# Kernel tuning notes

Hardware: AMD Instinct MI355X
Metric: run time of the kernel (lower is better)

## Reference

```python
import jax, jax.numpy as jnp
import numpy as np

T, H, E, I, TOP_K = 2048, 1024, 8, 2048, 2
SOFTCAP = 30.0


def setup_inputs() -> dict:
    key = jax.random.key(0)
    k1, k2, k3, k4, k5 = jax.random.split(key, 5)
    scale_h = 1.0 / np.sqrt(H)
    scale_i = 1.0 / np.sqrt(I)
    return {
        "hidden_states": jax.random.normal(k1, (T, H), dtype=jnp.float32),
        "gate_w": jax.random.normal(k2, (H, E), dtype=jnp.float32) * scale_h,
        "wg": jax.random.normal(k3, (E, H, I), dtype=jnp.float32) * scale_h,
        "wu": jax.random.normal(k4, (E, H, I), dtype=jnp.float32) * scale_h,
        "wd": jax.random.normal(k5, (E, I, H), dtype=jnp.float32) * scale_i,
    }


def reference(hidden_states, gate_w, wg, wu, wd):
    # Router: fp32 linear gate, then softcap: logits/cap -> tanh (as in source)
    router_logits = hidden_states @ gate_w                      # [T, E]
    router_logits = jnp.tanh(router_logits / SOFTCAP)

    # Top-k routing: softmax over the selected top-k logits (renormalized)
    topk_vals, topk_idx = jax.lax.top_k(router_logits, TOP_K)    # [T, K]
    topk_probs = jax.nn.softmax(topk_vals, axis=-1)              # [T, K]
    # Dense combine weights [T, E], zero for unselected experts
    weights = jnp.zeros((T, E), dtype=hidden_states.dtype)
    weights = weights.at[jnp.arange(T)[:, None], topk_idx].set(topk_probs)

    # Grouped expert MLP (gated, gelu): out_e = gelu(x@wg_e) * (x@wu_e) @ wd_e
    g = jnp.einsum("th,ehi->tei", hidden_states, wg)             # [T, E, I]
    u = jnp.einsum("th,ehi->tei", hidden_states, wu)             # [T, E, I]
    act = jax.nn.gelu(g) * u                                     # [T, E, I]
    expert_out = jnp.einsum("tei,eih->teh", act, wd)             # [T, E, H]

    # Weighted combine across experts
    return jnp.einsum("te,teh->th", weights, expert_out)         # [T, H]
```

## Files before the change

kernel.cpp:

```cpp
#include <hip/hip_runtime.h>
#include <hip/hip_bf16.h>

#define TT 2048
#define HD 1024
#define NE 8
#define ID 2048

typedef short bf16x8 __attribute__((ext_vector_type(8)));
typedef float f32x4 __attribute__((ext_vector_type(4)));

__device__ __forceinline__ unsigned f2bf(float f){
  unsigned u = __float_as_uint(f);
  return (u + 0x7FFFu + ((u >> 16) & 1u)) >> 16;
}
__device__ __forceinline__ float gelu_t(float x){
  float x3 = x * x * x;
  return 0.5f * x * (1.f + tanhf(0.7978845608028654f * (x + 0.044715f * x3)));
}

typedef const __attribute__((address_space(1))) unsigned int as1_uint;
typedef __attribute__((address_space(3))) unsigned int as3_uint;
__device__ __forceinline__ void gll16(const unsigned short* g, unsigned short* l) {
  __builtin_amdgcn_global_load_lds((as1_uint*)g, (as3_uint*)l, 16, 0, 0);
}

__global__ __launch_bounds__(64) void router_kernel(
    const float* __restrict__ x, const float* __restrict__ gw,
    int* __restrict__ counts, int* __restrict__ list_ak, float* __restrict__ wlist)
{
  int t = blockIdx.x;
  int lane = threadIdx.x;
  float acc[NE];
  #pragma unroll
  for (int e = 0; e < NE; ++e) acc[e] = 0.f;
  const float* xr = x + (size_t)t * HD;
  #pragma unroll
  for (int j = 0; j < HD / 64; ++j) {
    int h = j * 64 + lane;
    float xv = xr[h];
    float4 g0 = *(const float4*)(gw + (size_t)h * NE);
    float4 g1 = *(const float4*)(gw + (size_t)h * NE + 4);
    acc[0] += xv * g0.x; acc[1] += xv * g0.y;
    acc[2] += xv * g0.z; acc[3] += xv * g0.w;
    acc[4] += xv * g1.x; acc[5] += xv * g1.y;
    acc[6] += xv * g1.z; acc[7] += xv * g1.w;
  }
  #pragma unroll
  for (int e = 0; e < NE; ++e) {
    float v = acc[e];
    #pragma unroll
    for (int off = 32; off > 0; off >>= 1) v += __shfl_xor(v, off, 64);
    acc[e] = v;
  }
  if (lane == 0) {
    float lg[NE];
    #pragma unroll
    for (int e = 0; e < NE; ++e) lg[e] = tanhf(acc[e] * (1.0f / 30.0f));
    int i0 = 0;
    #pragma unroll
    for (int e = 1; e < NE; ++e) if (lg[e] > lg[i0]) i0 = e;
    int i1 = (i0 == 0) ? 1 : 0;
    #pragma unroll
    for (int e = 0; e < NE; ++e) if (e != i0 && lg[e] > lg[i1]) i1 = e;
    float e1 = __expf(lg[i1] - lg[i0]);
    float w0 = 1.f / (1.f + e1);
    float w1 = 1.f - w0;
    int p0 = atomicAdd(counts + i0, 1);
    list_ak[i0 * TT + p0] = t * 2;
    wlist[i0 * TT + p0] = w0;
    int p1 = atomicAdd(counts + i1, 1);
    list_ak[i1 * TT + p1] = t * 2 + 1;
    wlist[i1 * TT + p1] = w1;
  }
}

__global__ void xcvt_kernel(const float* __restrict__ x, unsigned short* __restrict__ xb)
{
  int i = blockIdx.x * blockDim.x + threadIdx.x;
  const float* p = x + (size_t)i * 8;
  float4 v0 = *(const float4*)p;
  float4 v1 = *(const float4*)(p + 4);
  uint4 o;
  o.x = f2bf(v0.x) | (f2bf(v0.y) << 16);
  o.y = f2bf(v0.z) | (f2bf(v0.w) << 16);
  o.z = f2bf(v1.x) | (f2bf(v1.y) << 16);
  o.w = f2bf(v1.z) | (f2bf(v1.w) << 16);
  *(uint4*)(xb + (size_t)i * 8) = o;
}

__global__ __launch_bounds__(256) void tcvt_kernel(
    const float* __restrict__ in, unsigned short* __restrict__ out, int R, int C)
{
  __shared__ float tile[64 * 66];
  int e = blockIdx.z;
  const float* inp = in + (size_t)e * R * C;
  unsigned short* outp = out + (size_t)e * R * C;
  int r0 = blockIdx.y * 64, c0 = blockIdx.x * 64;
  int tid = threadIdx.x;
  int lr = tid >> 4, lc = (tid & 15) * 4;
  #pragma unroll
  for (int i = 0; i < 4; ++i) {
    float4 v = *(const float4*)(inp + (size_t)(r0 + i * 16 + lr) * C + c0 + lc);
    float* tp = &tile[(i * 16 + lr) * 66 + lc];
    tp[0] = v.x; tp[1] = v.y; tp[2] = v.z; tp[3] = v.w;
  }
  __syncthreads();
  int oc = tid >> 2, os = (tid & 3) * 16;
  unsigned short* op = outp + (size_t)(c0 + oc) * R + r0 + os;
  uint4 o[2];
  unsigned* ow = (unsigned*)o;
  #pragma unroll
  for (int m = 0; m < 8; ++m) {
    float a = tile[(os + 2 * m) * 66 + oc];
    float b = tile[(os + 2 * m + 1) * 66 + oc];
    ow[m] = f2bf(a) | (f2bf(b) << 16);
  }
  *(uint4*)op = o[0];
  *(uint4*)(op + 8) = o[1];
}

#define BK 32


__global__ __launch_bounds__(256, 4) void gu_gemm(
    const unsigned short* __restrict__ xb,
    const unsigned short* __restrict__ wgT,
    const unsigned short* __restrict__ wuT,
    unsigned short* __restrict__ act,
    const int* __restrict__ counts, const int* __restrict__ list_ak)
{
  int e = blockIdx.z;
  int nCnt = counts[e];
  int m0 = blockIdx.y * 64;
  if (m0 >= nCnt) return;
  int c0 = blockIdx.x * 128;
  const unsigned short* Wg = wgT + (size_t)e * HD * ID;
  const unsigned short* Wu = wuT + (size_t)e * HD * ID;

  __shared__ __align__(16) unsigned short As[2][64 * BK];
  __shared__ __align__(16) unsigned short Bg[2][128 * BK];
  __shared__ __align__(16) unsigned short Bu[2][128 * BK];

  int tid = threadIdx.x;
  int wave = tid >> 6, lane = tid & 63;
  int wn = wave * 32;

  int arow = wave * 16 + (lane >> 2);
  int gpos = m0 + arow; if (gpos >= nCnt) gpos = nCnt - 1;
  int usw = ((lane & 3) ^ ((lane >> 3) & 3)) * 8;
  const unsigned short* aptr =
      xb + (size_t)(list_ak[e * TT + gpos] >> 1) * HD + usw;
  int aldso = wave * 512;

  int colL = wave * 16 + (lane >> 2);
  const unsigned short* bg0 = Wg + (size_t)(c0 + colL) * HD + usw;
  const unsigned short* bu0 = Wu + (size_t)(c0 + colL) * HD + usw;
  const size_t bstep = (size_t)64 * HD;
  int ldso = wave * 512;

  auto stage = [&](int k0, int b) {
    gll16(aptr + k0,         &As[b][aldso]);
    gll16(bg0 + k0,          &Bg[b][ldso]);
    gll16(bg0 + k0 + bstep,  &Bg[b][ldso + 2048]);
    gll16(bu0 + k0,          &Bu[b][ldso]);
    gll16(bu0 + k0 + bstep,  &Bu[b][ldso + 2048]);
  };

  f32x4 accg[4][2], accu[4][2];
  f32x4 zed = {0.f, 0.f, 0.f, 0.f};
  #pragma unroll
  for (int i = 0; i < 4; ++i)
    #pragma unroll
    for (int j = 0; j < 2; ++j) { accg[i][j] = zed; accu[i][j] = zed; }

  stage(0, 0);

  int q = lane >> 4, l15 = lane & 15;
  int bswz = (q ^ ((l15 >> 1) & 3)) * 8;

  for (int k0 = 0; k0 < HD; k0 += BK) {
    int cur = (k0 >> 5) & 1;
    if (k0 + BK < HD) {
      stage(k0 + BK, cur ^ 1);
      asm volatile("s_waitcnt vmcnt(5)" ::: "memory");
    } else {
      asm volatile("s_waitcnt vmcnt(0)" ::: "memory");
    }
    __builtin_amdgcn_s_barrier();

    bf16x8 af[4];
    #pragma unroll
    for (int mt = 0; mt < 4; ++mt) {
      int r = mt * 16 + l15;
      af[mt] = *(const bf16x8*)(&As[cur][r * BK + ((q ^ ((r >> 1) & 3)) * 8)]);
    }
    #pragma unroll
    for (int nt = 0; nt < 2; ++nt) {
      int col = wn + nt * 16 + l15;
      bf16x8 bgf  = *(const bf16x8*)(&Bg[cur][col * BK + bswz]);
      bf16x8 buf_ = *(const bf16x8*)(&Bu[cur][col * BK + bswz]);
      #pragma unroll
      for (int mt = 0; mt < 4; ++mt) {
        accg[mt][nt] = __builtin_amdgcn_mfma_f32_16x16x32_bf16(af[mt], bgf,  accg[mt][nt], 0, 0, 0);
        accu[mt][nt] = __builtin_amdgcn_mfma_f32_16x16x32_bf16(af[mt], buf_, accu[mt][nt], 0, 0, 0);
      }
    }
    asm volatile("s_waitcnt lgkmcnt(0)" ::: "memory");
    __builtin_amdgcn_s_barrier();
  }

  int cc = lane & 15, rg = lane >> 4;
  #pragma unroll
  for (int mt = 0; mt < 4; ++mt) {
    #pragma unroll
    for (int r = 0; r < 4; ++r) {
      int pos = m0 + mt * 16 + rg * 4 + r;
      if (pos >= nCnt) continue;
      int ak = list_ak[e * TT + pos];
      #pragma unroll
      for (int nt = 0; nt < 2; ++nt) {
        int ncol = c0 + wn + nt * 16 + cc;
        float avl = gelu_t(accg[mt][nt][r]) * accu[mt][nt][r];
        act[(size_t)ak * ID + ncol] = (unsigned short)f2bf(avl);
      }
    }
  }
}

__global__ __launch_bounds__(256, 5) void d_gemm(
    const unsigned short* __restrict__ act,
    const unsigned short* __restrict__ wdT,
    float* __restrict__ yw,
    const int* __restrict__ counts, const int* __restrict__ list_ak,
    const float* __restrict__ wlist)
{
  int e = blockIdx.z;
  int nCnt = counts[e];
  int m0 = (blockIdx.y >> 1) * 64;
  int ks = blockIdx.y & 1;
  if (m0 >= nCnt) return;
  int c0 = blockIdx.x * 128;
  const unsigned short* Wd = wdT + (size_t)e * ID * HD;

  __shared__ __align__(16) unsigned short As[2][64 * BK];
  __shared__ __align__(16) unsigned short Bt[2][128 * BK];

  int tid = threadIdx.x;
  int wave = tid >> 6, lane = tid & 63;
  int wn = wave * 32;

  int arow = wave * 16 + (lane >> 2);
  int gpos = m0 + arow; if (gpos >= nCnt) gpos = nCnt - 1;
  int usw = ((lane & 3) ^ ((lane >> 3) & 3)) * 8;
  const unsigned short* aptr =
      act + (size_t)list_ak[e * TT + gpos] * ID + ks * 1024 + usw;
  int aldso = wave * 512;

  int colL = wave * 16 + (lane >> 2);
  const unsigned short* bp0 = Wd + (size_t)(c0 + colL) * ID + ks * 1024 + usw;
  const size_t bstep = (size_t)64 * ID;
  int ldso = wave * 512;

  auto stage = [&](int k0, int b) {
    gll16(aptr + k0,        &As[b][aldso]);
    gll16(bp0 + k0,         &Bt[b][ldso]);
    gll16(bp0 + k0 + bstep, &Bt[b][ldso + 2048]);
  };

  f32x4 acc[4][2];
  f32x4 zed = {0.f, 0.f, 0.f, 0.f};
  #pragma unroll
  for (int i = 0; i < 4; ++i)
    #pragma unroll
    for (int j = 0; j < 2; ++j) acc[i][j] = zed;

  stage(0, 0);

  int q = lane >> 4, l15 = lane & 15;
  int bswz = (q ^ ((l15 >> 1) & 3)) * 8;

  for (int k0 = 0; k0 < 1024; k0 += BK) {
    int cur = (k0 >> 5) & 1;
    if (k0 + BK < 1024) {
      stage(k0 + BK, cur ^ 1);
      asm volatile("s_waitcnt vmcnt(3)" ::: "memory");
    } else {
      asm volatile("s_waitcnt vmcnt(0)" ::: "memory");
    }
    __builtin_amdgcn_s_barrier();

    bf16x8 af[4], bf[2];
    #pragma unroll
    for (int mt = 0; mt < 4; ++mt) {
      int r = mt * 16 + l15;
      af[mt] = *(const bf16x8*)(&As[cur][r * BK + ((q ^ ((r >> 1) & 3)) * 8)]);
    }
    #pragma unroll
    for (int nt = 0; nt < 2; ++nt) {
      int col = wn + nt * 16 + l15;
      bf[nt] = *(const bf16x8*)(&Bt[cur][col * BK + bswz]);
    }
    #pragma unroll
    for (int mt = 0; mt < 4; ++mt)
      #pragma unroll
      for (int nt = 0; nt < 2; ++nt)
        acc[mt][nt] = __builtin_amdgcn_mfma_f32_16x16x32_bf16(af[mt], bf[nt], acc[mt][nt], 0, 0, 0);

    asm volatile("s_waitcnt lgkmcnt(0)" ::: "memory");
    __builtin_amdgcn_s_barrier();
  }

  int cc = lane & 15, rg = lane >> 4;
  #pragma unroll
  for (int mt = 0; mt < 4; ++mt) {
    #pragma unroll
    for (int r = 0; r < 4; ++r) {
      int pos = m0 + mt * 16 + rg * 4 + r;
      if (pos >= nCnt) continue;
      int ak = list_ak[e * TT + pos];
      float wsc = wlist[e * TT + pos];
      #pragma unroll
      for (int nt = 0; nt < 2; ++nt) {
        int ncol = c0 + wn + nt * 16 + cc;
        yw[((size_t)ks * (TT * 2) + ak) * HD + ncol] = acc[mt][nt][r] * wsc;
      }
    }
  }
}

__global__ void combine_kernel(const float* __restrict__ yw, float* __restrict__ out)
{
  const int total = TT * HD / 4;
  const size_t S = (size_t)TT * 2 * HD;
  for (int i = blockIdx.x * blockDim.x + threadIdx.x; i < total;
       i += gridDim.x * blockDim.x) {
    int i4 = i * 4;
    int t = i4 >> 10;
    int h = i4 & (HD - 1);
    float4 a = *(const float4*)(yw + (size_t)(2 * t) * HD + h);
    float4 b = *(const float4*)(yw + (size_t)(2 * t + 1) * HD + h);
    float4 c = *(const float4*)(yw + S + (size_t)(2 * t) * HD + h);
    float4 d = *(const float4*)(yw + S + (size_t)(2 * t + 1) * HD + h);
    float4 o;
    o.x = a.x + b.x + c.x + d.x;
    o.y = a.y + b.y + c.y + d.y;
    o.z = a.z + b.z + c.z + d.z;
    o.w = a.w + b.w + c.w + d.w;
    *(float4*)(out + (size_t)i4) = o;
  }
}

extern "C" void kernel_launch(void* const* d_in, const int* in_sizes, int n_in,
                              void* d_out, int out_size, void* d_ws, size_t ws_size,
                              hipStream_t stream) {
  const float* x  = (const float*)d_in[0];
  const float* gw = (const float*)d_in[1];
  const float* wg = (const float*)d_in[2];
  const float* wu = (const float*)d_in[3];
  const float* wd = (const float*)d_in[4];
  float* out = (float*)d_out;

  char* ws = (char*)d_ws;
  int* counts   = (int*)ws;
  int* list_ak  = (int*)(ws + 256);
  float* wlist  = (float*)(ws + 256 + 65536);
  size_t off = 256 + 2 * 65536;
  unsigned short* xb  = (unsigned short*)(ws + off); off += (size_t)TT * HD * 2;
  unsigned short* act = (unsigned short*)(ws + off); off += (size_t)TT * 2 * ID * 2;
  float* yw           = (float*)(ws + off);          off += (size_t)2 * TT * 2 * HD * 4;
  unsigned short* wgT = (unsigned short*)(ws + off); off += (size_t)NE * HD * ID * 2;
  unsigned short* wuT = (unsigned short*)(ws + off); off += (size_t)NE * HD * ID * 2;
  unsigned short* wdT = (unsigned short*)(ws + off);

  (void)hipMemsetAsync(counts, 0, 256, stream);
  router_kernel<<<TT, 64, 0, stream>>>(x, gw, counts, list_ak, wlist);
  xcvt_kernel<<<TT * HD / 8 / 256, 256, 0, stream>>>(x, xb);

  tcvt_kernel<<<dim3(ID / 64, HD / 64, NE), 256, 0, stream>>>(wg, wgT, HD, ID);
  tcvt_kernel<<<dim3(ID / 64, HD / 64, NE), 256, 0, stream>>>(wu, wuT, HD, ID);
  tcvt_kernel<<<dim3(HD / 64, ID / 64, NE), 256, 0, stream>>>(wd, wdT, ID, HD);

  dim3 blk(256);
  dim3 gGU(ID / 128, 32, NE);
  gu_gemm<<<gGU, blk, 0, stream>>>(xb, wgT, wuT, act, counts, list_ak);

  dim3 gD(HD / 128, 64, NE);
  d_gemm<<<gD, blk, 0, stream>>>(act, wdT, yw, counts, list_ak, wlist);

  combine_kernel<<<1024, 256, 0, stream>>>(yw, out);
}
```

Baseline: 396.8 us.

## Load expert weights directly to registers and use persistent row-strided GEMM blocks

Both expert GEMMs stop staging weight tiles through shared memory. Each wave now loads its B fragments straight from global memory into registers, one k-step ahead, and only the gathered activation rows go through LDS. The grid is reshaped to (expert, 8 or 16 slots, column tiles), and each block loops over row tiles with stride 512 instead of exiting early on empty tiles, which cuts idle blocks and LDS use. The cost is that weight loads are no longer shared across waves through LDS and are strided 16-byte global reads that rely on the caches. The column-tile-major launch order may also change L2 reuse of weights. The d_gemm occupancy hint also drops from 5 to 4.

```diff
diff --git a/kernel.cpp b/kernel.cpp
--- a/kernel.cpp
+++ b/kernel.cpp
@@ -129,200 +129,192 @@
     unsigned short* __restrict__ act,
     const int* __restrict__ counts, const int* __restrict__ list_ak)
 {
-  int e = blockIdx.z;
+  int e = blockIdx.x;
   int nCnt = counts[e];
-  int m0 = blockIdx.y * 64;
-  if (m0 >= nCnt) return;
-  int c0 = blockIdx.x * 128;
+  int c0 = blockIdx.z * 128;
   const unsigned short* Wg = wgT + (size_t)e * HD * ID;
   const unsigned short* Wu = wuT + (size_t)e * HD * ID;
 
   __shared__ __align__(16) unsigned short As[2][64 * BK];
-  __shared__ __align__(16) unsigned short Bg[2][128 * BK];
-  __shared__ __align__(16) unsigned short Bu[2][128 * BK];
 
   int tid = threadIdx.x;
   int wave = tid >> 6, lane = tid & 63;
   int wn = wave * 32;
-
-  int arow = wave * 16 + (lane >> 2);
-  int gpos = m0 + arow; if (gpos >= nCnt) gpos = nCnt - 1;
+  int q = lane >> 4, l15 = lane & 15;
   int usw = ((lane & 3) ^ ((lane >> 3) & 3)) * 8;
-  const unsigned short* aptr =
-      xb + (size_t)(list_ak[e * TT + gpos] >> 1) * HD + usw;
   int aldso = wave * 512;
-
-  int colL = wave * 16 + (lane >> 2);
-  const unsigned short* bg0 = Wg + (size_t)(c0 + colL) * HD + usw;
-  const unsigned short* bu0 = Wu + (size_t)(c0 + colL) * HD + usw;
-  const size_t bstep = (size_t)64 * HD;
-  int ldso = wave * 512;
-
-  auto stage = [&](int k0, int b) {
-    gll16(aptr + k0,         &As[b][aldso]);
-    gll16(bg0 + k0,          &Bg[b][ldso]);
-    gll16(bg0 + k0 + bstep,  &Bg[b][ldso + 2048]);
-    gll16(bu0 + k0,          &Bu[b][ldso]);
-    gll16(bu0 + k0 + bstep,  &Bu[b][ldso + 2048]);
-  };
-
-  f32x4 accg[4][2], accu[4][2];
-  f32x4 zed = {0.f, 0.f, 0.f, 0.f};
-  #pragma unroll
-  for (int i = 0; i < 4; ++i)
-    #pragma unroll
-    for (int j = 0; j < 2; ++j) { accg[i][j] = zed; accu[i][j] = zed; }
-
-  stage(0, 0);
-
-  int q = lane >> 4, l15 = lane & 15;
-  int bswz = (q ^ ((l15 >> 1) & 3)) * 8;
-
-  for (int k0 = 0; k0 < HD; k0 += BK) {
-    int cur = (k0 >> 5) & 1;
-    if (k0 + BK < HD) {
-      stage(k0 + BK, cur ^ 1);
-      asm volatile("s_waitcnt vmcnt(5)" ::: "memory");
-    } else {
-      asm volatile("s_waitcnt vmcnt(0)" ::: "memory");
-    }
-    __builtin_amdgcn_s_barrier();
-
-    bf16x8 af[4];
+  int afsw = (q ^ ((l15 >> 1) & 3)) * 8;
+
+  const unsigned short* pBg = Wg + (size_t)(c0 + wn + l15) * HD + q * 8;
+  const unsigned short* pBu = Wu + (size_t)(c0 + wn + l15) * HD + q * 8;
+  const size_t ntstep = (size_t)16 * HD;
+
+  for (int m0 = blockIdx.y * 64; m0 < nCnt; m0 += 8 * 64) {
+    int gpos = m0 + wave * 16 + (lane >> 2);
+    if (gpos >= nCnt) gpos = nCnt - 1;
+    const unsigned short* aptr =
+        xb + (size_t)(list_ak[e * TT + gpos] >> 1) * HD + usw;
+
+    f32x4 accg[4][2], accu[4][2];
+    f32x4 zed = {0.f, 0.f, 0.f, 0.f};
+    #pragma unroll
+    for (int i = 0; i < 4; ++i)
+      #pragma unroll
+      for (int j = 0; j < 2; ++j) { accg[i][j] = zed; accu[i][j] = zed; }
+
+    bf16x8 bgf[2], buf_[2];
+    gll16(aptr, &As[0][aldso]);
+    #pragma unroll
+    for (int nt = 0; nt < 2; ++nt) {
+      bgf[nt]  = *(const bf16x8*)(pBg + nt * ntstep);
+      buf_[nt] = *(const bf16x8*)(pBu + nt * ntstep);
+    }
+    asm volatile("" ::: "memory");
+
+    for (int k0 = 0; k0 < HD; k0 += BK) {
+      int cur = (k0 >> 5) & 1;
+      int nk = k0 + BK;
+      if (nk < HD) {
+        gll16(aptr + nk, &As[cur ^ 1][aldso]);
+        asm volatile("s_waitcnt vmcnt(1)" ::: "memory");
+      } else {
+        asm volatile("s_waitcnt vmcnt(0)" ::: "memory");
+      }
+      __builtin_amdgcn_s_barrier();
+
+      bf16x8 af[4];
+      #pragma unroll
+      for (int mt = 0; mt < 4; ++mt)
+        af[mt] = *(const bf16x8*)(&As[cur][(mt * 16 + l15) * BK + afsw]);
+
+      #pragma unroll
+      for (int nt = 0; nt < 2; ++nt) {
+        bf16x8 bg = bgf[nt], bu = buf_[nt];
+        #pragma unroll
+        for (int mt = 0; mt < 4; ++mt) {
+          accg[mt][nt] = __builtin_amdgcn_mfma_f32_16x16x32_bf16(af[mt], bg, accg[mt][nt], 0, 0, 0);
+          accu[mt][nt] = __builtin_amdgcn_mfma_f32_16x16x32_bf16(af[mt], bu, accu[mt][nt], 0, 0, 0);
+        }
+        if (nk < HD) {
+          bgf[nt]  = *(const bf16x8*)(pBg + nt * ntstep + nk);
+          buf_[nt] = *(const bf16x8*)(pBu + nt * ntstep + nk);
+        }
+      }
+      asm volatile("s_waitcnt lgkmcnt(0)" ::: "memory");
+      asm volatile("" ::: "memory");
+      __builtin_amdgcn_s_barrier();
+    }
+
+    int cc = lane & 15, rg = lane >> 4;
     #pragma unroll
     for (int mt = 0; mt < 4; ++mt) {
-      int r = mt * 16 + l15;
-      af[mt] = *(const bf16x8*)(&As[cur][r * BK + ((q ^ ((r >> 1) & 3)) * 8)]);
-    }
-    #pragma unroll
-    for (int nt = 0; nt < 2; ++nt) {
-      int col = wn + nt * 16 + l15;
-      bf16x8 bgf  = *(const bf16x8*)(&Bg[cur][col * BK + bswz]);
-      bf16x8 buf_ = *(const bf16x8*)(&Bu[cur][col * BK + bswz]);
-      #pragma unroll
-      for (int mt = 0; mt < 4; ++mt) {
-        accg[mt][nt] = __builtin_amdgcn_mfma_f32_16x16x32_bf16(af[mt], bgf,  accg[mt][nt], 0, 0, 0);
-        accu[mt][nt] = __builtin_amdgcn_mfma_f32_16x16x32_bf16(af[mt], buf_, accu[mt][nt], 0, 0, 0);
-      }
-    }
-    asm volatile("s_waitcnt lgkmcnt(0)" ::: "memory");
-    __builtin_amdgcn_s_barrier();
-  }
-
-  int cc = lane & 15, rg = lane >> 4;
-  #pragma unroll
-  for (int mt = 0; mt < 4; ++mt) {
-    #pragma unroll
-    for (int r = 0; r < 4; ++r) {
-      int pos = m0 + mt * 16 + rg * 4 + r;
-      if (pos >= nCnt) continue;
-      int ak = list_ak[e * TT + pos];
-      #pragma unroll
-      for (int nt = 0; nt < 2; ++nt) {
-        int ncol = c0 + wn + nt * 16 + cc;
-        float avl = gelu_t(accg[mt][nt][r]) * accu[mt][nt][r];
-        act[(size_t)ak * ID + ncol] = (unsigned short)f2bf(avl);
-      }
-    }
-  }
-}
-
-__global__ __launch_bounds__(256, 5) void d_gemm(
+      #pragma unroll
+      for (int r = 0; r < 4; ++r) {
+        int pos = m0 + mt * 16 + rg * 4 + r;
+        if (pos >= nCnt) continue;
+        int ak = list_ak[e * TT + pos];
+        #pragma unroll
+        for (int nt = 0; nt < 2; ++nt) {
+          int ncol = c0 + wn + nt * 16 + cc;
+          float avl = gelu_t(accg[mt][nt][r]) * accu[mt][nt][r];
+          act[(size_t)ak * ID + ncol] = (unsigned short)f2bf(avl);
+        }
+      }
+    }
+  }
+}
+
+__global__ __launch_bounds__(256, 4) void d_gemm(
     const unsigned short* __restrict__ act,
     const unsigned short* __restrict__ wdT,
     float* __restrict__ yw,
     const int* __restrict__ counts, const int* __restrict__ list_ak,
     const float* __restrict__ wlist)
 {
-  int e = blockIdx.z;
+  int e = blockIdx.x;
   int nCnt = counts[e];
-  int m0 = (blockIdx.y >> 1) * 64;
+  int mslot = blockIdx.y >> 1;
   int ks = blockIdx.y & 1;
-  if (m0 >= nCnt) return;
-  int c0 = blockIdx.x * 128;
+  int c0 = blockIdx.z * 128;
   const unsigned short* Wd = wdT + (size_t)e * ID * HD;
 
   __shared__ __align__(16) unsigned short As[2][64 * BK];
-  __shared__ __align__(16) unsigned short Bt[2][128 * BK];
 
   int tid = threadIdx.x;
   int wave = tid >> 6, lane = tid & 63;
   int wn = wave * 32;
-
-  int arow = wave * 16 + (lane >> 2);
-  int gpos = m0 + arow; if (gpos >= nCnt) gpos = nCnt - 1;
+  int q = lane >> 4, l15 = lane & 15;
   int usw = ((lane & 3) ^ ((lane >> 3) & 3)) * 8;
-  const unsigned short* aptr =
-      act + (size_t)list_ak[e * TT + gpos] * ID + ks * 1024 + usw;
   int aldso = wave * 512;
-
-  int colL = wave * 16 + (lane >> 2);
-  const unsigned short* bp0 = Wd + (size_t)(c0 + colL) * ID + ks * 1024 + usw;
-  const size_t bstep = (size_t)64 * ID;
-  int ldso = wave * 512;
-
-  auto stage = [&](int k0, int b) {
-    gll16(aptr + k0,        &As[b][aldso]);
-    gll16(bp0 + k0,         &Bt[b][ldso]);
-    gll16(bp0 + k0 + bstep, &Bt[b][ldso + 2048]);
-  };
-
-  f32x4 acc[4][2];
-  f32x4 zed = {0.f, 0.f, 0.f, 0.f};
-  #pragma unroll
-  for (int i = 0; i < 4; ++i)
-    #pragma unroll
-    for (int j = 0; j < 2; ++j) acc[i][j] = zed;
-
-  stage(0, 0);
-
-  int q = lane >> 4, l15 = lane & 15;
-  int bswz = (q ^ ((l15 >> 1) & 3)) * 8;
-
-  for (int k0 = 0; k0 < 1024; k0 += BK) {
-    int cur = (k0 >> 5) & 1;
-    if (k0 + BK < 1024) {
-      stage(k0 + BK, cur ^ 1);
-      asm volatile("s_waitcnt vmcnt(3)" ::: "memory");
-    } else {
-      asm volatile("s_waitcnt vmcnt(0)" ::: "memory");
-    }
-    __builtin_amdgcn_s_barrier();
-
-    bf16x8 af[4], bf[2];
+  int afsw = (q ^ ((l15 >> 1) & 3)) * 8;
+
+  const unsigned short* pB = Wd + (size_t)(c0 + wn + l15) * ID + ks * 1024 + q * 8;
+  const size_t ntstep = (size_t)16 * ID;
+
+  for (int m0 = mslot * 64; m0 < nCnt; m0 += 8 * 64) {
+    int gpos = m0 + wave * 16 + (lane >> 2);
+    if (gpos >= nCnt) gpos = nCnt - 1;
+    const unsigned short* aptr =
+        act + (size_t)list_ak[e * TT + gpos] * ID + ks * 1024 + usw;
+
+    f32x4 acc[4][2];
+    f32x4 zed = {0.f, 0.f, 0.f, 0.f};
+    #pragma unroll
+    for (int i = 0; i < 4; ++i)
+      #pragma unroll
+      for (int j = 0; j < 2; ++j) acc[i][j] = zed;
+
+    bf16x8 bf[2];
+    gll16(aptr, &As[0][aldso]);
+    #pragma unroll
+    for (int nt = 0; nt < 2; ++nt)
+      bf[nt] = *(const bf16x8*)(pB + nt * ntstep);
+    asm volatile("" ::: "memory");
+
+    for (int k0 = 0; k0 < 1024; k0 += BK) {
+      int cur = (k0 >> 5) & 1;
+      int nk = k0 + BK;
+      if (nk < 1024) {
+        gll16(aptr + nk, &As[cur ^ 1][aldso]);
+        asm volatile("s_waitcnt vmcnt(1)" ::: "memory");
+      } else {
+        asm volatile("s_waitcnt vmcnt(0)" ::: "memory");
+      }
+      __builtin_amdgcn_s_barrier();
+
+      bf16x8 af[4];
+      #pragma unroll
+      for (int mt = 0; mt < 4; ++mt)
+        af[mt] = *(const bf16x8*)(&As[cur][(mt * 16 + l15) * BK + afsw]);
+
+      #pragma unroll
+      for (int nt = 0; nt < 2; ++nt) {
+        bf16x8 b = bf[nt];
+        #pragma unroll
+        for (int mt = 0; mt < 4; ++mt)
+          acc[mt][nt] = __builtin_amdgcn_mfma_f32_16x16x32_bf16(af[mt], b, acc[mt][nt], 0, 0, 0);
+        if (nk < 1024)
+          bf[nt] = *(const bf16x8*)(pB + nt * ntstep + nk);
+      }
+      asm volatile("s_waitcnt lgkmcnt(0)" ::: "memory");
+      asm volatile("" ::: "memory");
+      __builtin_amdgcn_s_barrier();
+    }
+
+    int cc = lane & 15, rg = lane >> 4;
     #pragma unroll
     for (int mt = 0; mt < 4; ++mt) {
-      int r = mt * 16 + l15;
-      af[mt] = *(const bf16x8*)(&As[cur][r * BK + ((q ^ ((r >> 1) & 3)) * 8)]);
-    }
-    #pragma unroll
-    for (int nt = 0; nt < 2; ++nt) {
-      int col = wn + nt * 16 + l15;
-      bf[nt] = *(const bf16x8*)(&Bt[cur][col * BK + bswz]);
-    }
-    #pragma unroll
-    for (int mt = 0; mt < 4; ++mt)
-      #pragma unroll
-      for (int nt = 0; nt < 2; ++nt)
-        acc[mt][nt] = __builtin_amdgcn_mfma_f32_16x16x32_bf16(af[mt], bf[nt], acc[mt][nt], 0, 0, 0);
-
-    asm volatile("s_waitcnt lgkmcnt(0)" ::: "memory");
-    __builtin_amdgcn_s_barrier();
-  }
-
-  int cc = lane & 15, rg = lane >> 4;
-  #pragma unroll
-  for (int mt = 0; mt < 4; ++mt) {
-    #pragma unroll
-    for (int r = 0; r < 4; ++r) {
-      int pos = m0 + mt * 16 + rg * 4 + r;
-      if (pos >= nCnt) continue;
-      int ak = list_ak[e * TT + pos];
-      float wsc = wlist[e * TT + pos];
-      #pragma unroll
-      for (int nt = 0; nt < 2; ++nt) {
-        int ncol = c0 + wn + nt * 16 + cc;
-        yw[((size_t)ks * (TT * 2) + ak) * HD + ncol] = acc[mt][nt][r] * wsc;
+      #pragma unroll
+      for (int r = 0; r < 4; ++r) {
+        int pos = m0 + mt * 16 + rg * 4 + r;
+        if (pos >= nCnt) continue;
+        int ak = list_ak[e * TT + pos];
+        float wsc = wlist[e * TT + pos];
+        #pragma unroll
+        for (int nt = 0; nt < 2; ++nt) {
+          int ncol = c0 + wn + nt * 16 + cc;
+          yw[((size_t)ks * (TT * 2) + ak) * HD + ncol] = acc[mt][nt][r] * wsc;
+        }
       }
     }
   }
@@ -381,10 +373,10 @@
   tcvt_kernel<<<dim3(HD / 64, ID / 64, NE), 256, 0, stream>>>(wd, wdT, ID, HD);
 
   dim3 blk(256);
-  dim3 gGU(ID / 128, 32, NE);
+  dim3 gGU(NE, 8, ID / 128);
   gu_gemm<<<gGU, blk, 0, stream>>>(xb, wgT, wuT, act, counts, list_ak);
 
-  dim3 gD(HD / 128, 64, NE);
+  dim3 gD(NE, 16, HD / 128);
   d_gemm<<<gD, blk, 0, stream>>>(act, wdT, yw, counts, list_ak, wlist);
 
   combine_kernel<<<1024, 256, 0, stream>>>(yw, out);
```

Result: slower. 492.1 us (+24.0%).

## Grow expert GEMM M-tile to 128 rows with 8-wave blocks

Applied to the files above, without the earlier changes.

Both expert GEMMs now use 512-thread blocks arranged as a 2x4 wave grid. Each block covers 128 token rows instead of 64, so every weight tile staged into LDS is reused by twice as many rows and weight traffic per output drops. The grid's row dimension is halved and each wave issues fewer staged loads per K step, with the vmcnt waits adjusted to match. In exchange there are fewer blocks per expert, more wasted rows on partial tiles, and larger LDS and register demand per block, which may lower occupancy.

```diff
diff --git a/kernel.cpp b/kernel.cpp
--- a/kernel.cpp
+++ b/kernel.cpp
@@ -120,9 +120,10 @@
 }
 
 #define BK 32
-
-
-__global__ __launch_bounds__(256, 4) void gu_gemm(
+#define BM 128
+
+
+__global__ __launch_bounds__(512, 4) void gu_gemm(
     const unsigned short* __restrict__ xb,
     const unsigned short* __restrict__ wgT,
     const unsigned short* __restrict__ wuT,
@@ -131,39 +132,35 @@
 {
   int e = blockIdx.z;
   int nCnt = counts[e];
-  int m0 = blockIdx.y * 64;
+  int m0 = blockIdx.y * BM;
   if (m0 >= nCnt) return;
   int c0 = blockIdx.x * 128;
   const unsigned short* Wg = wgT + (size_t)e * HD * ID;
   const unsigned short* Wu = wuT + (size_t)e * HD * ID;
 
-  __shared__ __align__(16) unsigned short As[2][64 * BK];
+  __shared__ __align__(16) unsigned short As[2][BM * BK];
   __shared__ __align__(16) unsigned short Bg[2][128 * BK];
   __shared__ __align__(16) unsigned short Bu[2][128 * BK];
 
   int tid = threadIdx.x;
   int wave = tid >> 6, lane = tid & 63;
-  int wn = wave * 32;
-
-  int arow = wave * 16 + (lane >> 2);
-  int gpos = m0 + arow; if (gpos >= nCnt) gpos = nCnt - 1;
+  int wm = wave >> 2, wnq = wave & 3;
+  int q = lane >> 4, l15 = lane & 15;
   int usw = ((lane & 3) ^ ((lane >> 3) & 3)) * 8;
+  int fsw = (q ^ ((l15 >> 1) & 3)) * 8;
+
+  int srow = wave * 16 + (lane >> 2);
+  int gpos = m0 + srow; if (gpos >= nCnt) gpos = nCnt - 1;
   const unsigned short* aptr =
       xb + (size_t)(list_ak[e * TT + gpos] >> 1) * HD + usw;
-  int aldso = wave * 512;
-
-  int colL = wave * 16 + (lane >> 2);
-  const unsigned short* bg0 = Wg + (size_t)(c0 + colL) * HD + usw;
-  const unsigned short* bu0 = Wu + (size_t)(c0 + colL) * HD + usw;
-  const size_t bstep = (size_t)64 * HD;
-  int ldso = wave * 512;
+  const unsigned short* bgp = Wg + (size_t)(c0 + srow) * HD + usw;
+  const unsigned short* bup = Wu + (size_t)(c0 + srow) * HD + usw;
+  int so = wave * 512;
 
   auto stage = [&](int k0, int b) {
-    gll16(aptr + k0,         &As[b][aldso]);
-    gll16(bg0 + k0,          &Bg[b][ldso]);
-    gll16(bg0 + k0 + bstep,  &Bg[b][ldso + 2048]);
-    gll16(bu0 + k0,          &Bu[b][ldso]);
-    gll16(bu0 + k0 + bstep,  &Bu[b][ldso + 2048]);
+    gll16(aptr + k0, &As[b][so]);
+    gll16(bgp + k0,  &Bg[b][so]);
+    gll16(bup + k0,  &Bu[b][so]);
   };
 
   f32x4 accg[4][2], accu[4][2];
@@ -174,15 +171,12 @@
     for (int j = 0; j < 2; ++j) { accg[i][j] = zed; accu[i][j] = zed; }
 
   stage(0, 0);
-
-  int q = lane >> 4, l15 = lane & 15;
-  int bswz = (q ^ ((l15 >> 1) & 3)) * 8;
 
   for (int k0 = 0; k0 < HD; k0 += BK) {
     int cur = (k0 >> 5) & 1;
     if (k0 + BK < HD) {
       stage(k0 + BK, cur ^ 1);
-      asm volatile("s_waitcnt vmcnt(5)" ::: "memory");
+      asm volatile("s_waitcnt vmcnt(3)" ::: "memory");
     } else {
       asm volatile("s_waitcnt vmcnt(0)" ::: "memory");
     }
@@ -190,15 +184,13 @@
 
     bf16x8 af[4];
     #pragma unroll
-    for (int mt = 0; mt < 4; ++mt) {
-      int r = mt * 16 + l15;
-      af[mt] = *(const bf16x8*)(&As[cur][r * BK + ((q ^ ((r >> 1) & 3)) * 8)]);
-    }
+    for (int mt = 0; mt < 4; ++mt)
+      af[mt] = *(const bf16x8*)(&As[cur][(wm * 64 + mt * 16 + l15) * BK + fsw]);
     #pragma unroll
     for (int nt = 0; nt < 2; ++nt) {
-      int col = wn + nt * 16 + l15;
-      bf16x8 bgf  = *(const bf16x8*)(&Bg[cur][col * BK + bswz]);
-      bf16x8 buf_ = *(const bf16x8*)(&Bu[cur][col * BK + bswz]);
+      int col = wnq * 32 + nt * 16 + l15;
+      bf16x8 bgf  = *(const bf16x8*)(&Bg[cur][col * BK + fsw]);
+      bf16x8 buf_ = *(const bf16x8*)(&Bu[cur][col * BK + fsw]);
       #pragma unroll
       for (int mt = 0; mt < 4; ++mt) {
         accg[mt][nt] = __builtin_amdgcn_mfma_f32_16x16x32_bf16(af[mt], bgf,  accg[mt][nt], 0, 0, 0);
@@ -209,17 +201,17 @@
     __builtin_amdgcn_s_barrier();
   }
 
-  int cc = lane & 15, rg = lane >> 4;
+  int cc = l15, rg = q;
   #pragma unroll
   for (int mt = 0; mt < 4; ++mt) {
     #pragma unroll
     for (int r = 0; r < 4; ++r) {
-      int pos = m0 + mt * 16 + rg * 4 + r;
+      int pos = m0 + wm * 64 + mt * 16 + rg * 4 + r;
       if (pos >= nCnt) continue;
       int ak = list_ak[e * TT + pos];
       #pragma unroll
       for (int nt = 0; nt < 2; ++nt) {
-        int ncol = c0 + wn + nt * 16 + cc;
+        int ncol = c0 + wnq * 32 + nt * 16 + cc;
         float avl = gelu_t(accg[mt][nt][r]) * accu[mt][nt][r];
         act[(size_t)ak * ID + ncol] = (unsigned short)f2bf(avl);
       }
@@ -227,7 +219,7 @@
   }
 }
 
-__global__ __launch_bounds__(256, 5) void d_gemm(
+__global__ __launch_bounds__(512, 4) void d_gemm(
     const unsigned short* __restrict__ act,
     const unsigned short* __restrict__ wdT,
     float* __restrict__ yw,
@@ -236,35 +228,33 @@
 {
   int e = blockIdx.z;
   int nCnt = counts[e];
-  int m0 = (blockIdx.y >> 1) * 64;
+  int m0 = (blockIdx.y >> 1) * BM;
   int ks = blockIdx.y & 1;
   if (m0 >= nCnt) return;
   int c0 = blockIdx.x * 128;
   const unsigned short* Wd = wdT + (size_t)e * ID * HD;
 
-  __shared__ __align__(16) unsigned short As[2][64 * BK];
+  __shared__ __align__(16) unsigned short As[2][BM * BK];
   __shared__ __align__(16) unsigned short Bt[2][128 * BK];
 
   int tid = threadIdx.x;
   int wave = tid >> 6, lane = tid & 63;
-  int wn = wave * 32;
-
-  int arow = wave * 16 + (lane >> 2);
-  int gpos = m0 + arow; if (gpos >= nCnt) gpos = nCnt - 1;
+  int wm = wave >> 2, wnq = wave & 3;
+  int q = lane >> 4, l15 = lane & 15;
   int usw = ((lane & 3) ^ ((lane >> 3) & 3)) * 8;
+  int fsw = (q ^ ((l15 >> 1) & 3)) * 8;
+
+  int srow = wave * 16 + (lane >> 2);
+  int gpos = m0 + srow; if (gpos >= nCnt) gpos = nCnt - 1;
   const unsigned short* aptr =
       act + (size_t)list_ak[e * TT + gpos] * ID + ks * 1024 + usw;
-  int aldso = wave * 512;
-
-  int colL = wave * 16 + (lane >> 2);
-  const unsigned short* bp0 = Wd + (size_t)(c0 + colL) * ID + ks * 1024 + usw;
-  const size_t bstep = (size_t)64 * ID;
-  int ldso = wave * 512;
+  const unsigned short* bp =
+      Wd + (size_t)(c0 + srow) * ID + ks * 1024 + usw;
+  int so = wave * 512;
 
   auto stage = [&](int k0, int b) {
-    gll16(aptr + k0,        &As[b][aldso]);
-    gll16(bp0 + k0,         &Bt[b][ldso]);
-    gll16(bp0 + k0 + bstep, &Bt[b][ldso + 2048]);
+    gll16(aptr + k0, &As[b][so]);
+    gll16(bp + k0,   &Bt[b][so]);
   };
 
   f32x4 acc[4][2];
@@ -275,15 +265,12 @@
     for (int j = 0; j < 2; ++j) acc[i][j] = zed;
 
   stage(0, 0);
-
-  int q = lane >> 4, l15 = lane & 15;
-  int bswz = (q ^ ((l15 >> 1) & 3)) * 8;
 
   for (int k0 = 0; k0 < 1024; k0 += BK) {
     int cur = (k0 >> 5) & 1;
     if (k0 + BK < 1024) {
       stage(k0 + BK, cur ^ 1);
-      asm volatile("s_waitcnt vmcnt(3)" ::: "memory");
+      asm volatile("s_waitcnt vmcnt(2)" ::: "memory");
     } else {
       asm volatile("s_waitcnt vmcnt(0)" ::: "memory");
     }
@@ -291,14 +278,12 @@
 
     bf16x8 af[4], bf[2];
     #pragma unroll
-    for (int mt = 0; mt < 4; ++mt) {
-      int r = mt * 16 + l15;
-      af[mt] = *(const bf16x8*)(&As[cur][r * BK + ((q ^ ((r >> 1) & 3)) * 8)]);
-    }
+    for (int mt = 0; mt < 4; ++mt)
+      af[mt] = *(const bf16x8*)(&As[cur][(wm * 64 + mt * 16 + l15) * BK + fsw]);
     #pragma unroll
     for (int nt = 0; nt < 2; ++nt) {
-      int col = wn + nt * 16 + l15;
-      bf[nt] = *(const bf16x8*)(&Bt[cur][col * BK + bswz]);
+      int col = wnq * 32 + nt * 16 + l15;
+      bf[nt] = *(const bf16x8*)(&Bt[cur][col * BK + fsw]);
     }
     #pragma unroll
     for (int mt = 0; mt < 4; ++mt)
@@ -310,18 +295,18 @@
     __builtin_amdgcn_s_barrier();
   }
 
-  int cc = lane & 15, rg = lane >> 4;
+  int cc = l15, rg = q;
   #pragma unroll
   for (int mt = 0; mt < 4; ++mt) {
     #pragma unroll
     for (int r = 0; r < 4; ++r) {
-      int pos = m0 + mt * 16 + rg * 4 + r;
+      int pos = m0 + wm * 64 + mt * 16 + rg * 4 + r;
       if (pos >= nCnt) continue;
       int ak = list_ak[e * TT + pos];
       float wsc = wlist[e * TT + pos];
       #pragma unroll
       for (int nt = 0; nt < 2; ++nt) {
-        int ncol = c0 + wn + nt * 16 + cc;
+        int ncol = c0 + wnq * 32 + nt * 16 + cc;
         yw[((size_t)ks * (TT * 2) + ak) * HD + ncol] = acc[mt][nt][r] * wsc;
       }
     }
@@ -380,11 +365,11 @@
   tcvt_kernel<<<dim3(ID / 64, HD / 64, NE), 256, 0, stream>>>(wu, wuT, HD, ID);
   tcvt_kernel<<<dim3(HD / 64, ID / 64, NE), 256, 0, stream>>>(wd, wdT, ID, HD);
 
-  dim3 blk(256);
-  dim3 gGU(ID / 128, 32, NE);
+  dim3 blk(512);
+  dim3 gGU(ID / 128, 16, NE);
   gu_gemm<<<gGU, blk, 0, stream>>>(xb, wgT, wuT, act, counts, list_ak);
 
-  dim3 gD(HD / 128, 64, NE);
+  dim3 gD(HD / 128, 32, NE);
   d_gemm<<<gD, blk, 0, stream>>>(act, wdT, yw, counts, list_ak, wlist);
 
   combine_kernel<<<1024, 256, 0, stream>>>(yw, out);
```

After: 381.1 us. 1.04x faster.
